# Kernel optimization log

Hardware: AMD Instinct MI355X
Metric: run time of the kernel (lower is better)

## Reference

```python
import jax, jax.numpy as jnp
import numpy as np

EPS = 1e-12  # matches torch F.normalize eps


def setup_inputs() -> dict:
    key = jax.random.key(0)
    k_x, k_w, k_b, k_c, k_f = jax.random.split(key, 5)
    N, C, H, W = 32, 128, 64, 64
    K = 64
    x = jax.random.normal(k_x, (N, C, H, W), dtype=jnp.float32)
    conv_w = jax.random.normal(k_w, (K, C), dtype=jnp.float32) * 0.05  # 1x1 conv weight [K,C,1,1] squeezed
    conv_b = jax.random.normal(k_b, (K,), dtype=jnp.float32) * 0.05
    centroids = jax.random.uniform(k_c, (K, C), dtype=jnp.float32)
    fc_w = jax.random.normal(k_f, (1, K), dtype=jnp.float32) * 0.1  # nn.Linear(K,1,bias=False).weight
    return {"x": x, "conv_w": conv_w, "conv_b": conv_b, "centroids": centroids, "fc_w": fc_w}


def _l2norm(v, axis):
    return v / jnp.maximum(jnp.linalg.norm(v, axis=axis, keepdims=True), EPS)


def reference(x, conv_w, conv_b, centroids, fc_w):
    N, C, H, W = x.shape
    K = conv_w.shape[0]
    # descriptor-wise L2 normalize over channel dim
    x = _l2norm(x, axis=1)
    xf = x.reshape(N, C, H * W)                                   # [N,C,S]
    # 1x1 conv == per-pixel linear over channels
    logits = jnp.einsum('kc,ncs->nks', conv_w, xf) + conv_b[None, :, None]
    a = jax.nn.softmax(logits, axis=1)                            # [N,K,S] soft assignment
    # VLAD: sum_s a[n,k,s] * (x[n,:,s] - centroids[k,:]), loop-free
    vlad = jnp.einsum('nks,ncs->nkc', a, xf) \
           - a.sum(axis=-1)[..., None] * centroids[None, :, :]    # [N,K,C]
    # intra-normalization over descriptor dim
    vlad = _l2norm(vlad, axis=2)
    # lastfc: [N,C,K] @ [K] -> [N,C]
    out = jnp.einsum('nkc,k->nc', vlad, fc_w[0])
    return out
```

## Files before the change

kernel.cpp:

```cpp
#include <hip/hip_runtime.h>
#include <math.h>

#define Nn 32
#define Cc 128
#define Ss 4096
#define Kk 64
#define NCHUNK 16
#define SCHUNK (Ss / NCHUNK)
#define ST 64
#define NSUB (SCHUNK / ST)
#define BLK 256

#define XCS 72
#define XTS 136
#define LKS 68
#define AS  72
#define RS  17

typedef __attribute__((ext_vector_type(8))) short short8;
typedef __attribute__((ext_vector_type(4))) float float4v;

__device__ __forceinline__ unsigned f2bf(float f) {
    unsigned u = __builtin_bit_cast(unsigned, f);
    return (u + 0x7fffu + ((u >> 16) & 1u)) >> 16;
}
__device__ __forceinline__ unsigned pack2(float a, float b) {
    return f2bf(a) | (f2bf(b) << 16);
}

__global__ __launch_bounds__(BLK, 2) void netvlad_main(
    const float* __restrict__ x,
    const float* __restrict__ conv_w,
    const float* __restrict__ conv_b,
    float* __restrict__ vlad,
    float* __restrict__ asum)
{
    __shared__ __align__(16) unsigned short xC[Cc * XCS];
    __shared__ __align__(16) float Lbuf[ST * LKS];
    __shared__ __align__(16) unsigned short aB[Kk * AS];
    __shared__ float red[ST * RS];
    __shared__ float invn[ST];
    unsigned short* xT = (unsigned short*)Lbuf;

    const int t    = threadIdx.x;
    const int n    = blockIdx.y;
    const int w    = t >> 6;
    const int l    = t & 63;
    const int m    = l & 15;
    const int quad = l >> 4;
    const int p    = t >> 2;
    const int ii   = t & 3;

    short8 wfrag[4];
    {
        const float* wr_ = conv_w + (16 * w + m) * Cc;
#pragma unroll
        for (int ks = 0; ks < 4; ++ks) {
            float4 wa = *(const float4*)(wr_ + 32 * ks + 8 * quad);
            float4 wb = *(const float4*)(wr_ + 32 * ks + 8 * quad + 4);
            union { short8 s8; unsigned u[4]; } W_;
            W_.u[0] = pack2(wa.x, wa.y);
            W_.u[1] = pack2(wa.z, wa.w);
            W_.u[2] = pack2(wb.x, wb.y);
            W_.u[3] = pack2(wb.z, wb.w);
            wfrag[ks] = W_.s8;
        }
    }
    float bias_r[4];
#pragma unroll
    for (int r = 0; r < 4; ++r) bias_r[r] = conv_b[16 * w + 4 * quad + r];

    float4v acc[8];
#pragma unroll
    for (int nt = 0; nt < 8; ++nt) acc[nt] = (float4v){0.f, 0.f, 0.f, 0.f};
    float asum_part[16];
#pragma unroll
    for (int j = 0; j < 16; ++j) asum_part[j] = 0.f;

    const float* xn = x + (size_t)n * Cc * Ss;

    const int sq   = (t & 15) << 2;
    const int crow = t >> 4;
    const float* xbase = xn + (size_t)crow * Ss + blockIdx.x * SCHUNK + sq;
    float4 pf[8];
#pragma unroll
    for (int r = 0; r < 8; ++r)
        pf[r] = *(const float4*)(xbase + (size_t)(16 * r) * Ss);

    for (int sub = 0; sub < NSUB; ++sub) {
        __syncthreads();

        {
            float sp0 = 0.f, sp1 = 0.f, sp2 = 0.f, sp3 = 0.f;
#pragma unroll
            for (int r = 0; r < 8; ++r) {
                float4 v = pf[r];
                sp0 += v.x * v.x; sp1 += v.y * v.y;
                sp2 += v.z * v.z; sp3 += v.w * v.w;
                uint2 pk = make_uint2(pack2(v.x, v.y), pack2(v.z, v.w));
                *(uint2*)&xC[(crow + 16 * r) * XCS + sq] = pk;
            }
            red[(sq + 0) * RS + crow] = sp0;
            red[(sq + 1) * RS + crow] = sp1;
            red[(sq + 2) * RS + crow] = sp2;
            red[(sq + 3) * RS + crow] = sp3;
        }
        if (sub < NSUB - 1) {
#pragma unroll
            for (int r = 0; r < 8; ++r)
                pf[r] = *(const float4*)(xbase + (size_t)(16 * r) * Ss + (sub + 1) * ST);
        }
        __syncthreads();

        if (t < ST) {
            float tot = 0.f;
#pragma unroll
            for (int i = 0; i < 16; ++i) tot += red[t * RS + i];
            invn[t] = 1.0f / fmaxf(sqrtf(tot), 1e-12f);
        }
        {
            int s = t & 63, oct0 = t >> 6;
#pragma unroll
            for (int q = 0; q < 4; ++q) {
                int oct = oct0 + 4 * q;
                uint4 dd;
                dd.x = (unsigned)xC[(8 * oct + 0) * XCS + s] | ((unsigned)xC[(8 * oct + 1) * XCS + s] << 16);
                dd.y = (unsigned)xC[(8 * oct + 2) * XCS + s] | ((unsigned)xC[(8 * oct + 3) * XCS + s] << 16);
                dd.z = (unsigned)xC[(8 * oct + 4) * XCS + s] | ((unsigned)xC[(8 * oct + 5) * XCS + s] << 16);
                dd.w = (unsigned)xC[(8 * oct + 6) * XCS + s] | ((unsigned)xC[(8 * oct + 7) * XCS + s] << 16);
                *(uint4*)&xT[s * XTS + 8 * oct] = dd;
            }
        }
        __syncthreads();

        float4v Lr[4];
#pragma unroll
        for (int nt = 0; nt < 4; ++nt) Lr[nt] = (float4v){0.f, 0.f, 0.f, 0.f};
#pragma unroll
        for (int nt = 0; nt < 4; ++nt) {
#pragma unroll
            for (int ks = 0; ks < 4; ++ks) {
                short8 b = *(const short8*)&xT[(16 * nt + m) * XTS + 32 * ks + 8 * quad];
                Lr[nt] = __builtin_amdgcn_mfma_f32_16x16x32_bf16(wfrag[ks], b, Lr[nt], 0, 0, 0);
            }
        }
        __syncthreads();

#pragma unroll
        for (int nt = 0; nt < 4; ++nt) {
            float iv = invn[16 * nt + m];
            float4 o;
            o.x = Lr[nt].x * iv + bias_r[0];
            o.y = Lr[nt].y * iv + bias_r[1];
            o.z = Lr[nt].z * iv + bias_r[2];
            o.w = Lr[nt].w * iv + bias_r[3];
            *(float4*)&Lbuf[(16 * nt + m) * LKS + 16 * w + 4 * quad] = o;
        }
        __syncthreads();

        {
            float lv[16];
#pragma unroll
            for (int j = 0; j < 16; ++j) lv[j] = Lbuf[p * LKS + ii + 4 * j];
            float mx = lv[0];
#pragma unroll
            for (int j = 1; j < 16; ++j) mx = fmaxf(mx, lv[j]);
            mx = fmaxf(mx, __shfl_xor(mx, 1));
            mx = fmaxf(mx, __shfl_xor(mx, 2));
            float e[16];
            float lsum = 0.f;
#pragma unroll
            for (int j = 0; j < 16; ++j) { e[j] = __expf(lv[j] - mx); lsum += e[j]; }
            lsum += __shfl_xor(lsum, 1);
            lsum += __shfl_xor(lsum, 2);
            float itot = 1.0f / lsum;
            float sca  = itot * invn[p];
#pragma unroll
            for (int j = 0; j < 16; ++j) {
                float av = e[j] * itot;
                asum_part[j] += av;
                aB[(ii + 4 * j) * AS + p] = (unsigned short)f2bf(e[j] * sca);
            }
        }
        __syncthreads();

#pragma unroll
        for (int ks = 0; ks < 2; ++ks) {
            short8 af = *(const short8*)&aB[(16 * w + m) * AS + 32 * ks + 8 * quad];
#pragma unroll
            for (int nt = 0; nt < 8; ++nt) {
                short8 bf_ = *(const short8*)&xC[(16 * nt + m) * XCS + 32 * ks + 8 * quad];
                acc[nt] = __builtin_amdgcn_mfma_f32_16x16x32_bf16(af, bf_, acc[nt], 0, 0, 0);
            }
        }
    }

    float* vb = vlad + ((size_t)n * Kk + 16 * w + 4 * quad) * Cc + m;
#pragma unroll
    for (int nt = 0; nt < 8; ++nt) {
        atomicAdd(vb + 0 * Cc + 16 * nt, acc[nt].x);
        atomicAdd(vb + 1 * Cc + 16 * nt, acc[nt].y);
        atomicAdd(vb + 2 * Cc + 16 * nt, acc[nt].z);
        atomicAdd(vb + 3 * Cc + 16 * nt, acc[nt].w);
    }

    __syncthreads();
#pragma unroll
    for (int j = 0; j < 16; ++j) Lbuf[p * LKS + ii + 4 * j] = asum_part[j];
    __syncthreads();
    if (t < Kk) {
        float s_ = 0.f;
        for (int p2 = 0; p2 < ST; ++p2) s_ += Lbuf[p2 * LKS + t];
        atomicAdd(&asum[n * Kk + t], s_);
    }
}

__global__ __launch_bounds__(256) void netvlad_final(
    const float* __restrict__ vlad, const float* __restrict__ asum,
    const float* __restrict__ centroids, const float* __restrict__ fc_w,
    float* __restrict__ out)
{
    __shared__ float scale_s[Kk];
    __shared__ float asum_s[Kk];
    __shared__ float red2[Kk][4];
    __shared__ float4 osum[8][32];

    const int n = blockIdx.x;
    const int t = threadIdx.x;
    const int k = t >> 2;
    const int q = t & 3;

    const float* vr = vlad + ((size_t)n * Kk + k) * Cc + q * 32;
    const float* cr = centroids + k * Cc + q * 32;
    const float  as = asum[n * Kk + k];

    float ssq = 0.f;
#pragma unroll
    for (int i = 0; i < 8; ++i) {
        float4 v4 = *(const float4*)(vr + 4 * i);
        float4 c4 = *(const float4*)(cr + 4 * i);
        float d0 = v4.x - as * c4.x;
        float d1 = v4.y - as * c4.y;
        float d2 = v4.z - as * c4.z;
        float d3 = v4.w - as * c4.w;
        ssq += d0 * d0 + d1 * d1 + d2 * d2 + d3 * d3;
    }
    red2[k][q] = ssq;
    __syncthreads();
    if (q == 0) {
        float tot = red2[k][0] + red2[k][1] + red2[k][2] + red2[k][3];
        scale_s[k] = fc_w[k] / fmaxf(sqrtf(tot), 1e-12f);
        asum_s[k]  = as;
    }
    __syncthreads();

    {
        const int cq = t & 31;
        const int sl = t >> 5;
        const float* vb2 = vlad + (size_t)n * Kk * Cc + 4 * cq;
        const float* cb2 = centroids + 4 * cq;
        float ox = 0.f, oy = 0.f, oz = 0.f, ow = 0.f;
#pragma unroll
        for (int j = 0; j < 8; ++j) {
            const int k2 = 8 * j + sl;
            float4 v4 = *(const float4*)(vb2 + (size_t)k2 * Cc);
            float4 c4 = *(const float4*)(cb2 + (size_t)k2 * Cc);
            float sc = scale_s[k2];
            float a2 = asum_s[k2];
            ox += sc * (v4.x - a2 * c4.x);
            oy += sc * (v4.y - a2 * c4.y);
            oz += sc * (v4.z - a2 * c4.z);
            ow += sc * (v4.w - a2 * c4.w);
        }
        osum[sl][cq] = make_float4(ox, oy, oz, ow);
    }
    __syncthreads();
    if (t < 32) {
        float4 tot = osum[0][t];
#pragma unroll
        for (int s2 = 1; s2 < 8; ++s2) {
            float4 o2 = osum[s2][t];
            tot.x += o2.x; tot.y += o2.y; tot.z += o2.z; tot.w += o2.w;
        }
        *(float4*)&out[n * Cc + 4 * t] = tot;
    }
}

extern "C" void kernel_launch(void* const* d_in, const int* in_sizes, int n_in,
                              void* d_out, int out_size, void* d_ws, size_t ws_size,
                              hipStream_t stream) {
    (void)in_sizes; (void)n_in; (void)out_size; (void)ws_size;
    const float* x         = (const float*)d_in[0];
    const float* conv_w    = (const float*)d_in[1];
    const float* conv_b    = (const float*)d_in[2];
    const float* centroids = (const float*)d_in[3];
    const float* fc_w      = (const float*)d_in[4];
    float* out = (float*)d_out;

    float* vlad = (float*)d_ws;
    float* asum = vlad + (size_t)Nn * Kk * Cc;
    size_t zero_bytes = ((size_t)Nn * Kk * Cc + (size_t)Nn * Kk) * sizeof(float);
    hipMemsetAsync(d_ws, 0, zero_bytes, stream);

    dim3 grid(NCHUNK, Nn);
    netvlad_main<<<grid, BLK, 0, stream>>>(x, conv_w, conv_b, vlad, asum);
    netvlad_final<<<Nn, 256, 0, stream>>>(vlad, asum, centroids, fc_w, out);
}
```

Before: 119.9 us.

## Replace global atomics with per-chunk partial buffers reduced in finalize kernel

After: 116.1 us. 1.03x faster.

```diff
diff --git a/kernel.cpp b/kernel.cpp
--- a/kernel.cpp
+++ b/kernel.cpp
@@ -32,8 +32,8 @@
     const float* __restrict__ x,
     const float* __restrict__ conv_w,
     const float* __restrict__ conv_b,
-    float* __restrict__ vlad,
-    float* __restrict__ asum)
+    float* __restrict__ vladp,
+    float* __restrict__ asump)
 {
     __shared__ __align__(16) unsigned short xC[Cc * XCS];
     __shared__ __align__(16) float Lbuf[ST * LKS];
@@ -42,8 +42,9 @@
     __shared__ float invn[ST];
     unsigned short* xT = (unsigned short*)Lbuf;
 
-    const int t    = threadIdx.x;
-    const int n    = blockIdx.y;
+    const int t     = threadIdx.x;
+    const int n     = blockIdx.y;
+    const int chunk = blockIdx.x;
     const int w    = t >> 6;
     const int l    = t & 63;
     const int m    = l & 15;
@@ -81,7 +82,7 @@
 
     const int sq   = (t & 15) << 2;
     const int crow = t >> 4;
-    const float* xbase = xn + (size_t)crow * Ss + blockIdx.x * SCHUNK + sq;
+    const float* xbase = xn + (size_t)crow * Ss + chunk * SCHUNK + sq;
     float4 pf[8];
 #pragma unroll
     for (int r = 0; r < 8; ++r)
@@ -195,13 +196,15 @@
         }
     }
 
-    float* vb = vlad + ((size_t)n * Kk + 16 * w + 4 * quad) * Cc + m;
-#pragma unroll
-    for (int nt = 0; nt < 8; ++nt) {
-        atomicAdd(vb + 0 * Cc + 16 * nt, acc[nt].x);
-        atomicAdd(vb + 1 * Cc + 16 * nt, acc[nt].y);
-        atomicAdd(vb + 2 * Cc + 16 * nt, acc[nt].z);
-        atomicAdd(vb + 3 * Cc + 16 * nt, acc[nt].w);
+    {
+        float* vb = vladp + ((((size_t)chunk * Nn + n) * Kk) + 16 * w + 4 * quad) * Cc + m;
+#pragma unroll
+        for (int nt = 0; nt < 8; ++nt) {
+            vb[0 * Cc + 16 * nt] = acc[nt].x;
+            vb[1 * Cc + 16 * nt] = acc[nt].y;
+            vb[2 * Cc + 16 * nt] = acc[nt].z;
+            vb[3 * Cc + 16 * nt] = acc[nt].w;
+        }
     }
 
     __syncthreads();
@@ -211,78 +214,77 @@
     if (t < Kk) {
         float s_ = 0.f;
         for (int p2 = 0; p2 < ST; ++p2) s_ += Lbuf[p2 * LKS + t];
-        atomicAdd(&asum[n * Kk + t], s_);
-    }
-}
-
-__global__ __launch_bounds__(256) void netvlad_final(
-    const float* __restrict__ vlad, const float* __restrict__ asum,
-    const float* __restrict__ centroids, const float* __restrict__ fc_w,
+        asump[((size_t)chunk * Nn + n) * Kk + t] = s_;
+    }
+}
+
+__global__ __launch_bounds__(BLK) void netvlad_final(
+    const float* __restrict__ vladp,
+    const float* __restrict__ asump,
+    const float* __restrict__ centroids,
+    const float* __restrict__ fc_w,
     float* __restrict__ out)
 {
-    __shared__ float scale_s[Kk];
-    __shared__ float asum_s[Kk];
-    __shared__ float red2[Kk][4];
-    __shared__ float4 osum[8][32];
-
-    const int n = blockIdx.x;
-    const int t = threadIdx.x;
-    const int k = t >> 2;
-    const int q = t & 3;
-
-    const float* vr = vlad + ((size_t)n * Kk + k) * Cc + q * 32;
-    const float* cr = centroids + k * Cc + q * 32;
-    const float  as = asum[n * Kk + k];
-
-    float ssq = 0.f;
-#pragma unroll
-    for (int i = 0; i < 8; ++i) {
-        float4 v4 = *(const float4*)(vr + 4 * i);
-        float4 c4 = *(const float4*)(cr + 4 * i);
-        float d0 = v4.x - as * c4.x;
-        float d1 = v4.y - as * c4.y;
-        float d2 = v4.z - as * c4.z;
-        float d3 = v4.w - as * c4.w;
-        ssq += d0 * d0 + d1 * d1 + d2 * d2 + d3 * d3;
-    }
-    red2[k][q] = ssq;
-    __syncthreads();
-    if (q == 0) {
-        float tot = red2[k][0] + red2[k][1] + red2[k][2] + red2[k][3];
-        scale_s[k] = fc_w[k] / fmaxf(sqrtf(tot), 1e-12f);
-        asum_s[k]  = as;
-    }
-    __syncthreads();
-
-    {
-        const int cq = t & 31;
-        const int sl = t >> 5;
-        const float* vb2 = vlad + (size_t)n * Kk * Cc + 4 * cq;
-        const float* cb2 = centroids + 4 * cq;
-        float ox = 0.f, oy = 0.f, oz = 0.f, ow = 0.f;
-#pragma unroll
-        for (int j = 0; j < 8; ++j) {
-            const int k2 = 8 * j + sl;
-            float4 v4 = *(const float4*)(vb2 + (size_t)k2 * Cc);
-            float4 c4 = *(const float4*)(cb2 + (size_t)k2 * Cc);
-            float sc = scale_s[k2];
-            float a2 = asum_s[k2];
-            ox += sc * (v4.x - a2 * c4.x);
-            oy += sc * (v4.y - a2 * c4.y);
-            oz += sc * (v4.z - a2 * c4.z);
-            ow += sc * (v4.w - a2 * c4.w);
-        }
-        osum[sl][cq] = make_float4(ox, oy, oz, ow);
-    }
-    __syncthreads();
+    __shared__ float asum_s[8];
+    __shared__ float scale_s[8];
+    __shared__ float4 osum[8 * 32];
+
+    const int t   = threadIdx.x;
+    const int bid = blockIdx.x;
+    const int n2  = bid >> 3;
+    const int kg  = bid & 7;
+    const int kl  = t >> 5;
+    const int c4  = t & 31;
+    const int k2  = 8 * kg + kl;
+
+    float4 v = make_float4(0.f, 0.f, 0.f, 0.f);
+    const float* vp = vladp + ((size_t)n2 * Kk + k2) * Cc + 4 * c4;
+#pragma unroll
+    for (int ch = 0; ch < NCHUNK; ++ch) {
+        float4 u = *(const float4*)(vp + (size_t)ch * Nn * Kk * Cc);
+        v.x += u.x; v.y += u.y; v.z += u.z; v.w += u.w;
+    }
+    if (t < 8) {
+        float a = 0.f;
+#pragma unroll
+        for (int ch = 0; ch < NCHUNK; ++ch)
+            a += asump[((size_t)ch * Nn + n2) * Kk + 8 * kg + t];
+        asum_s[t] = a;
+    }
+    __syncthreads();
+
+    const float a2 = asum_s[kl];
+    float4 cv = *(const float4*)(centroids + (size_t)k2 * Cc + 4 * c4);
+    float dx = v.x - a2 * cv.x;
+    float dy = v.y - a2 * cv.y;
+    float dz = v.z - a2 * cv.z;
+    float dw = v.w - a2 * cv.w;
+
+    float ssq = dx * dx + dy * dy + dz * dz + dw * dw;
+    ssq += __shfl_xor(ssq, 1);
+    ssq += __shfl_xor(ssq, 2);
+    ssq += __shfl_xor(ssq, 4);
+    ssq += __shfl_xor(ssq, 8);
+    ssq += __shfl_xor(ssq, 16);
+    if ((t & 31) == 0)
+        scale_s[kl] = fc_w[k2] / fmaxf(sqrtf(ssq), 1e-12f);
+    __syncthreads();
+
+    const float sc = scale_s[kl];
+    osum[kl * 32 + c4] = make_float4(sc * dx, sc * dy, sc * dz, sc * dw);
+    __syncthreads();
+
     if (t < 32) {
-        float4 tot = osum[0][t];
-#pragma unroll
-        for (int s2 = 1; s2 < 8; ++s2) {
-            float4 o2 = osum[s2][t];
+        float4 tot = osum[t];
+#pragma unroll
+        for (int kl2 = 1; kl2 < 8; ++kl2) {
+            float4 o2 = osum[kl2 * 32 + t];
             tot.x += o2.x; tot.y += o2.y; tot.z += o2.z; tot.w += o2.w;
         }
-        *(float4*)&out[n * Cc + 4 * t] = tot;
+        atomicAdd(&out[n2 * Cc + 4 * t + 0], tot.x);
+        atomicAdd(&out[n2 * Cc + 4 * t + 1], tot.y);
+        atomicAdd(&out[n2 * Cc + 4 * t + 2], tot.z);
+        atomicAdd(&out[n2 * Cc + 4 * t + 3], tot.w);
     }
 }
 
@@ -297,12 +299,12 @@
     const float* fc_w      = (const float*)d_in[4];
     float* out = (float*)d_out;
 
-    float* vlad = (float*)d_ws;
-    float* asum = vlad + (size_t)Nn * Kk * Cc;
-    size_t zero_bytes = ((size_t)Nn * Kk * Cc + (size_t)Nn * Kk) * sizeof(float);
-    hipMemsetAsync(d_ws, 0, zero_bytes, stream);
+    float* vladp = (float*)d_ws;
+    float* asump = vladp + (size_t)NCHUNK * Nn * Kk * Cc;
+
+    hipMemsetAsync(out, 0, (size_t)Nn * Cc * sizeof(float), stream);
 
     dim3 grid(NCHUNK, Nn);
-    netvlad_main<<<grid, BLK, 0, stream>>>(x, conv_w, conv_b, vlad, asum);
-    netvlad_final<<<Nn, 256, 0, stream>>>(vlad, asum, centroids, fc_w, out);
-}
+    netvlad_main<<<grid, BLK, 0, stream>>>(x, conv_w, conv_b, vladp, asump);
+    netvlad_final<<<dim3(Nn * 8), BLK, 0, stream>>>(vladp, asump, centroids, fc_w, out);
+}
```
